# Kernel tuning notes

Measured on AMD Instinct MI355X. Metric: run time of the kernel, lower is better.

Reference implementation:

```python
import jax, jax.numpy as jnp
import numpy as np

N = 50000   # nodes
E = 800000  # edges
D = 128     # hidden_dim
O = 128     # out_dim (must equal hidden_dim; see prior_mean Linear)
T = 16      # number of timesteps for the modeled time encoding
EPS = 1e-9


def _gcn(x, W, b, src, dst, ew, n):
    """PyG-style GCNConv: add self-loops, symmetric deg^-1/2 normalization."""
    loop = jnp.arange(n)
    s = jnp.concatenate([src, loop])
    d = jnp.concatenate([dst, loop])
    w = jnp.concatenate([ew, jnp.ones((n,), x.dtype)])
    deg = jax.ops.segment_sum(w, d, num_segments=n)
    dinv = jnp.where(deg > 0, jax.lax.rsqrt(deg), 0.0)
    norm = dinv[s] * w * dinv[d]              # [E+N]
    h = x @ W                                  # [N, out]
    out = jax.ops.segment_sum(h[s] * norm[:, None], d, num_segments=n)
    return out + b


def setup_inputs() -> dict:
    key = jax.random.key(0)
    ks = jax.random.split(key, 20)

    def lin(k, fan_in, fan_out):
        return jax.random.normal(k, (fan_in, fan_out), jnp.float32) / np.sqrt(fan_in)

    return {
        "edge_index": jax.random.randint(ks[0], (2, E), 0, N, dtype=jnp.int64),
        "x": jax.random.normal(ks[1], (N, D), jnp.float32),
        "t": 3,
        "edge_score": jax.random.uniform(ks[2], (E,), jnp.float32),
        "total_len": 16,
        "train_len": 12,
        "W_enc": lin(ks[3], D, D), "b_enc": jnp.zeros((D,), jnp.float32),
        "W_mu": lin(ks[4], D, O), "b_mu": jnp.zeros((O,), jnp.float32),
        "W_std": lin(ks[5], D, O), "b_std": jnp.zeros((O,), jnp.float32),
        "W_prior": lin(ks[6], D, O), "b_prior": jnp.zeros((O,), jnp.float32),
        "W_pm": lin(ks[7], D, O), "b_pm": jnp.zeros((O,), jnp.float32),
        "W_ps": lin(ks[8], D, O), "b_ps": jnp.zeros((O,), jnp.float32),
        "time_emb": 0.02 * jax.random.normal(ks[9], (T, O), jnp.float32),
    }


def reference(edge_index, x, t, edge_score, total_len, train_len,
              W_enc, b_enc, W_mu, b_mu, W_std, b_std,
              W_prior, b_prior, W_pm, b_pm, W_ps, b_ps, time_emb):
    src, dst = edge_index[0], edge_index[1]
    n = x.shape[0]
    ones_e = jnp.ones((src.shape[0],), x.dtype)

    # encoder
    enc_t = jax.nn.relu(_gcn(x, W_enc, b_enc, src, dst, edge_score, n))
    # drop = 0.0 -> dropout is identity
    enc_mean_t = _gcn(enc_t, W_mu, b_mu, src, dst, ones_e, n)
    enc_std_t = jax.nn.sigmoid(_gcn(enc_t, W_std, b_std, src, dst, ones_e, n))

    # reparameterize (fixed eps for determinism)
    eps = jax.random.normal(jax.random.key(42), enc_mean_t.shape, enc_mean_t.dtype)
    conf_z_t = eps * enc_std_t + enc_mean_t

    # prior branch: time_encoding(prior, t) modeled as additive time embedding
    prior = jax.nn.relu(_gcn(x, W_prior, b_prior, src, dst, ones_e, n))
    prior = prior + time_emb[t]
    prior_mean = prior @ W_pm + b_pm
    prior_std = jax.nn.sigmoid(prior @ W_ps + b_ps)

    # fused KL divergence
    kl = (2.0 * jnp.log(prior_std + EPS) - 2.0 * jnp.log(enc_std_t + EPS)
          + ((enc_std_t + EPS) ** 2 + (enc_mean_t - prior_mean) ** 2)
          / (prior_std + EPS) ** 2 - 1.0)
    kl_loss = 0.5 * jnp.mean(jnp.sum(kl, axis=1), axis=0)
    return kl_loss, conf_z_t
```

## Files before the change

### kernel.cpp

```cpp
#include <hip/hip_runtime.h>
#include <math.h>

#define D 128

typedef unsigned int u32;
typedef unsigned short u16;
typedef __attribute__((ext_vector_type(8))) short bf16x8;
typedef __attribute__((ext_vector_type(4))) float f32x4;

__device__ __forceinline__ u32 rotl32(u32 x, int r){ return (x<<r) | (x>>(32-r)); }

__device__ __forceinline__ u16 f2bf(float x){
  u32 u = __float_as_uint(x);
  return (u16)((u + 0x7fffu + ((u >> 16) & 1u)) >> 16);
}
__device__ __forceinline__ float bf2f(u16 h){ return __uint_as_float(((u32)h) << 16); }

__device__ __forceinline__ float jax_normal_part_xor(u32 m){
  const u32 ks0 = 0u, ks1 = 42u, ks2 = 0x1BD11BF0u;
  u32 x0 = 0u + ks0;
  u32 x1 = m  + ks1;
  #define TF_R4(a,b,c,d) \
    x0 += x1; x1 = rotl32(x1,(a)); x1 ^= x0; \
    x0 += x1; x1 = rotl32(x1,(b)); x1 ^= x0; \
    x0 += x1; x1 = rotl32(x1,(c)); x1 ^= x0; \
    x0 += x1; x1 = rotl32(x1,(d)); x1 ^= x0;
  TF_R4(13,15,26,6)   x0 += ks1; x1 += ks2 + 1u;
  TF_R4(17,29,16,24)  x0 += ks2; x1 += ks0 + 2u;
  TF_R4(13,15,26,6)   x0 += ks0; x1 += ks1 + 3u;
  TF_R4(17,29,16,24)  x0 += ks1; x1 += ks2 + 4u;
  TF_R4(13,15,26,6)   x0 += ks2; x1 += ks0 + 5u;
  #undef TF_R4
  u32 bits = x0 ^ x1;
  float f = __uint_as_float((bits >> 9) | 0x3F800000u) - 1.0f;
  const float LO = -0.99999994f;
  float u = fmaxf(LO, f * 2.0f + LO);
  float w = -__logf(fmaf(-u, u, 1.0f));
  float p;
  if (w < 5.0f){
    w -= 2.5f;
    p =  2.81022636e-08f;
    p = fmaf(p, w,  3.43273939e-07f);
    p = fmaf(p, w, -3.5233877e-06f);
    p = fmaf(p, w, -4.39150654e-06f);
    p = fmaf(p, w,  0.00021858087f);
    p = fmaf(p, w, -0.00125372503f);
    p = fmaf(p, w, -0.00417768164f);
    p = fmaf(p, w,  0.246640727f);
    p = fmaf(p, w,  1.50140941f);
  } else {
    w = sqrtf(w) - 3.0f;
    p = -0.000200214257f;
    p = fmaf(p, w,  0.000100950558f);
    p = fmaf(p, w,  0.00134934322f);
    p = fmaf(p, w, -0.00367342844f);
    p = fmaf(p, w,  0.00573950773f);
    p = fmaf(p, w, -0.0076224613f);
    p = fmaf(p, w,  0.00943887047f);
    p = fmaf(p, w,  1.00167406f);
    p = fmaf(p, w,  2.83297682f);
  }
  return 1.41421354f * (p * u);
}

__device__ __forceinline__ float sigmoidf_(float z){ return 1.0f / (1.0f + __expf(-z)); }

__global__ __launch_bounds__(256) void k_eps(u32* __restrict__ epsb, int half_total){
  int idx = blockIdx.x*256 + threadIdx.x;
  int stride = gridDim.x*256;
  for (int i = idx; i < half_total; i += stride){
    u32 m0 = 2u*(u32)i;
    float e0 = jax_normal_part_xor(m0);
    float e1 = jax_normal_part_xor(m0 + 1u);
    epsb[i] = (u32)f2bf(e0) | ((u32)f2bf(e1) << 16);
  }
}

__global__ __launch_bounds__(256) void k_xconv(const float* __restrict__ x,
                                               u32* __restrict__ xb, int total2){
  int i = blockIdx.x*256 + threadIdx.x;
  if (i >= total2) return;
  float2 v = ((const float2*)x)[i];
  xb[i] = (u32)f2bf(v.x) | ((u32)f2bf(v.y) << 16);
}

__global__ void k_detect(const u32* __restrict__ e_u32, int* __restrict__ flag){
  __shared__ int s_nz;
  if (threadIdx.x == 0) s_nz = 0;
  __syncthreads();
  if (e_u32[2*threadIdx.x + 1] != 0u) atomicAdd(&s_nz, 1);
  __syncthreads();
  if (threadIdx.x == 0) *flag = (s_nz == 0) ? 1 : 0;
}

__global__ void k_init(int* __restrict__ cnt, int n){
  int i = blockIdx.x*256 + threadIdx.x;
  if (i < n) cnt[i] = 0;
}

__global__ void k_norm(const void* __restrict__ eidx, const int* __restrict__ flag,
                       int* __restrict__ src_w, int* __restrict__ dst_w,
                       int* __restrict__ cnt, int e){
  int i = blockIdx.x*256 + threadIdx.x;
  if (i >= e) return;
  int s, d;
  if (*flag){
    const u32* u = (const u32*)eidx;
    s = (int)u[2*(size_t)i];
    d = (int)u[2*((size_t)e + i)];
  } else {
    const int* p = (const int*)eidx;
    s = p[i];
    d = p[e + i];
  }
  src_w[i] = s;
  dst_w[i] = d;
  atomicAdd(&cnt[d], 1);
}

__global__ __launch_bounds__(256) void k_scan1(const int* __restrict__ cnt,
                                               int* __restrict__ rp,
                                               int* __restrict__ bsum, int n){
  __shared__ int sh[256];
  int tid = threadIdx.x, idx = blockIdx.x*256 + tid;
  int v = (idx < n) ? cnt[idx] : 0;
  sh[tid] = v; __syncthreads();
  for (int off = 1; off < 256; off <<= 1){
    int t = (tid >= off) ? sh[tid-off] : 0;
    __syncthreads(); sh[tid] += t; __syncthreads();
  }
  if (idx < n) rp[idx] = sh[tid] - v;
  if (tid == 255) bsum[blockIdx.x] = sh[255];
}

__global__ __launch_bounds__(1024) void k_scan2(int* __restrict__ bsum, int nb){
  __shared__ int sh[1024];
  int tid = threadIdx.x;
  int v = (tid < nb) ? bsum[tid] : 0;
  sh[tid] = v; __syncthreads();
  for (int off = 1; off < 1024; off <<= 1){
    int t = (tid >= off) ? sh[tid-off] : 0;
    __syncthreads(); sh[tid] += t; __syncthreads();
  }
  if (tid < nb) bsum[tid] = sh[tid] - v;
}

__global__ void k_scan3(int* __restrict__ rp, int* __restrict__ cur,
                        const int* __restrict__ bsum, const int* __restrict__ cnt,
                        float* __restrict__ dinv_o, int n, int e){
  int idx = blockIdx.x*256 + threadIdx.x;
  if (idx < n){
    int r = rp[idx] + bsum[blockIdx.x];
    rp[idx] = r; cur[idx] = r;
    dinv_o[idx] = rsqrtf((float)(cnt[idx] + 1));
  }
  if (idx == 0) rp[n] = e;
}

__global__ void k_scatter(const int* __restrict__ src, const int* __restrict__ dst,
                          const float* __restrict__ sc, int* __restrict__ cur,
                          int* __restrict__ col, float* __restrict__ wsrt, int e){
  int i = blockIdx.x*256 + threadIdx.x;
  if (i >= e) return;
  int d = dst[i];
  int p = atomicAdd(&cur[d], 1);
  col[p] = src[i];
  wsrt[p] = sc[i];
}

__global__ void k_deg(const int* __restrict__ rp, const float* __restrict__ wsrt,
                      float* __restrict__ dinv_s, int n){
  int i = blockIdx.x*256 + threadIdx.x;
  if (i >= n) return;
  float s = 1.0f;
  int e0 = rp[i], e1 = rp[i+1];
  for (int j = e0; j < e1; ++j) s += wsrt[j];
  dinv_s[i] = rsqrtf(s);
}

__global__ void k_wconv(const float* __restrict__ W0, const float* __restrict__ W1,
                        const float* __restrict__ W2, const float* __restrict__ W3,
                        const float* __restrict__ W4, const float* __restrict__ W5,
                        u16* __restrict__ wt){
  const float* Ws[6] = {W0,W1,W2,W3,W4,W5};
  const float* W = Ws[blockIdx.y];
  u16* Wt = wt + (size_t)blockIdx.y*16384;
  int idx = blockIdx.x*256 + threadIdx.x;
  int k = idx >> 7, col = idx & 127;
  Wt[col*128 + k] = f2bf(W[idx]);
}

__global__ __launch_bounds__(256) void k_agg_dual(
    const u32* __restrict__ xb, const int* __restrict__ rp,
    const int* __restrict__ col, const float* __restrict__ wsrt,
    const float* __restrict__ dinv_s, const float* __restrict__ dinv_o,
    u16* __restrict__ out_s, u16* __restrict__ out_o, int n){
  int wid = (blockIdx.x * 256 + threadIdx.x) >> 6;
  int lane = threadIdx.x & 63;
  if (wid >= n) return;
  float dsv = dinv_s[wid], dov = dinv_o[wid];
  u32 xv = xb[(size_t)wid*64 + lane];
  float xlo = bf2f((u16)(xv & 0xffff)), xhi = bf2f((u16)(xv >> 16));
  float ss = dsv*dsv, oo = dov*dov;
  float2 as = { xlo*ss, xhi*ss };
  float2 ao = { xlo*oo, xhi*oo };
  int e0 = rp[wid], e1 = rp[wid+1];
  for (int base = e0; base < e1; base += 64){
    int cnt = e1 - base; if (cnt > 64) cnt = 64;
    int idx = base + (lane < cnt ? lane : cnt - 1);
    int   sl = col[idx];
    float wl = wsrt[idx];
    float nsl = dinv_s[sl] * wl * dsv;
    float nol = dinv_o[sl] * dov;
    int j = 0;
    for (; j + 4 <= cnt; j += 4){
      int   s0=__shfl(sl,j),   s1=__shfl(sl,j+1),   s2=__shfl(sl,j+2),   s3=__shfl(sl,j+3);
      float a0=__shfl(nsl,j),  a1=__shfl(nsl,j+1),  a2=__shfl(nsl,j+2),  a3=__shfl(nsl,j+3);
      float b0=__shfl(nol,j),  b1=__shfl(nol,j+1),  b2=__shfl(nol,j+2),  b3=__shfl(nol,j+3);
      u32 r0 = xb[(size_t)s0*64 + lane];
      u32 r1 = xb[(size_t)s1*64 + lane];
      u32 r2 = xb[(size_t)s2*64 + lane];
      u32 r3 = xb[(size_t)s3*64 + lane];
      float l0 = bf2f((u16)(r0&0xffff)), h0 = bf2f((u16)(r0>>16));
      float l1 = bf2f((u16)(r1&0xffff)), h1 = bf2f((u16)(r1>>16));
      float l2 = bf2f((u16)(r2&0xffff)), h2 = bf2f((u16)(r2>>16));
      float l3 = bf2f((u16)(r3&0xffff)), h3 = bf2f((u16)(r3>>16));
      as.x = fmaf(a0,l0,as.x); as.y = fmaf(a0,h0,as.y);
      ao.x = fmaf(b0,l0,ao.x); ao.y = fmaf(b0,h0,ao.y);
      as.x = fmaf(a1,l1,as.x); as.y = fmaf(a1,h1,as.y);
      ao.x = fmaf(b1,l1,ao.x); ao.y = fmaf(b1,h1,ao.y);
      as.x = fmaf(a2,l2,as.x); as.y = fmaf(a2,h2,as.y);
      ao.x = fmaf(b2,l2,ao.x); ao.y = fmaf(b2,h2,ao.y);
      as.x = fmaf(a3,l3,as.x); as.y = fmaf(a3,h3,as.y);
      ao.x = fmaf(b3,l3,ao.x); ao.y = fmaf(b3,h3,ao.y);
    }
    for (; j < cnt; ++j){
      int   s0=__shfl(sl,j);
      float a0=__shfl(nsl,j), b0=__shfl(nol,j);
      u32 r0 = xb[(size_t)s0*64 + lane];
      float l0 = bf2f((u16)(r0&0xffff)), h0 = bf2f((u16)(r0>>16));
      as.x = fmaf(a0,l0,as.x); as.y = fmaf(a0,h0,as.y);
      ao.x = fmaf(b0,l0,ao.x); ao.y = fmaf(b0,h0,ao.y);
    }
  }
  ((u32*)out_s)[(size_t)wid*64 + lane] = (u32)f2bf(as.x) | ((u32)f2bf(as.y) << 16);
  ((u32*)out_o)[(size_t)wid*64 + lane] = (u32)f2bf(ao.x) | ((u32)f2bf(ao.y) << 16);
}

__global__ __launch_bounds__(256) void k_agg_one(
    const u16* __restrict__ h, const int* __restrict__ rp,
    const int* __restrict__ col, const float* __restrict__ dinv_o,
    u16* __restrict__ out, int n){
  int wid = (blockIdx.x * 256 + threadIdx.x) >> 6;
  int lane = threadIdx.x & 63;
  if (wid >= n) return;
  const u32* h2 = (const u32*)h;
  float dov = dinv_o[wid];
  u32 hv = h2[(size_t)wid*64 + lane];
  float oo = dov*dov;
  float2 ao = { bf2f((u16)(hv & 0xffff))*oo, bf2f((u16)(hv >> 16))*oo };
  int e0 = rp[wid], e1 = rp[wid+1];
  for (int base = e0; base < e1; base += 64){
    int cnt = e1 - base; if (cnt > 64) cnt = 64;
    int idx = base + (lane < cnt ? lane : cnt - 1);
    int   sl = col[idx];
    float nol = dinv_o[sl] * dov;
    int j = 0;
    for (; j + 4 <= cnt; j += 4){
      int   s0=__shfl(sl,j),  s1=__shfl(sl,j+1),  s2=__shfl(sl,j+2),  s3=__shfl(sl,j+3);
      float b0=__shfl(nol,j), b1=__shfl(nol,j+1), b2=__shfl(nol,j+2), b3=__shfl(nol,j+3);
      u32 r0 = h2[(size_t)s0*64 + lane];
      u32 r1 = h2[(size_t)s1*64 + lane];
      u32 r2 = h2[(size_t)s2*64 + lane];
      u32 r3 = h2[(size_t)s3*64 + lane];
      ao.x = fmaf(b0, bf2f((u16)(r0&0xffff)), ao.x); ao.y = fmaf(b0, bf2f((u16)(r0>>16)), ao.y);
      ao.x = fmaf(b1, bf2f((u16)(r1&0xffff)), ao.x); ao.y = fmaf(b1, bf2f((u16)(r1>>16)), ao.y);
      ao.x = fmaf(b2, bf2f((u16)(r2&0xffff)), ao.x); ao.y = fmaf(b2, bf2f((u16)(r2>>16)), ao.y);
      ao.x = fmaf(b3, bf2f((u16)(r3&0xffff)), ao.x); ao.y = fmaf(b3, bf2f((u16)(r3>>16)), ao.y);
    }
    for (; j < cnt; ++j){
      int   s0=__shfl(sl,j);
      float b0=__shfl(nol,j);
      u32 r0 = h2[(size_t)s0*64 + lane];
      ao.x = fmaf(b0, bf2f((u16)(r0&0xffff)), ao.x); ao.y = fmaf(b0, bf2f((u16)(r0>>16)), ao.y);
    }
  }
  ((u32*)out)[(size_t)wid*64 + lane] = (u32)f2bf(ao.x) | ((u32)f2bf(ao.y) << 16);
}


__global__ __launch_bounds__(256) void k_mfma_act2(
    const u16* __restrict__ A0, const u16* __restrict__ Wt0, const float* __restrict__ b0,
    const u16* __restrict__ A1, const u16* __restrict__ Wt1, const float* __restrict__ b1,
    const float* __restrict__ temb, const int* __restrict__ t_ptr,
    u16* __restrict__ out0, u16* __restrict__ out1, int n){
  const int sl = blockIdx.y;
  const u16* A  = sl ? A1 : A0;
  const u16* Wt = sl ? Wt1 : Wt0;
  const float* b = sl ? b1 : b0;
  u16* out = sl ? out1 : out0;
  const int tid = threadIdx.x;
  const int lane = tid & 63, wave = tid >> 6;
  const int lr = lane & 15, lg = lane >> 4;
  const int row0 = blockIdx.x * 16;
  int rowf = row0 + lr;
  int rowc = rowf < n ? rowf : n - 1;
  const char* Arow = (const char*)A + (size_t)rowc*256;
  const char* Wb   = (const char*)Wt + (wave*32 + lr)*256 + lg*16;
  f32x4 z = {0.f,0.f,0.f,0.f};
  f32x4 acc[2];
  acc[0] = z; acc[1] = z;
  #pragma unroll
  for (int ks = 0; ks < 4; ++ks){
    bf16x8 a = *(const bf16x8*)(Arow + ks*64 + lg*16);
    #pragma unroll
    for (int cf = 0; cf < 2; ++cf){
      bf16x8 bb = *(const bf16x8*)(Wb + cf*16*256 + ks*64);
      acc[cf] = __builtin_amdgcn_mfma_f32_16x16x32_bf16(a, bb, acc[cf], 0, 0, 0);
    }
  }
  int t = sl ? *t_ptr : 0;
  int rbase = row0 + (lg << 2);
  #pragma unroll
  for (int cf = 0; cf < 2; ++cf){
    int colw = wave*32 + cf*16 + lr;
    float bb = b[colw];
    float tt = sl ? temb[t*128 + colw] : 0.f;
    #pragma unroll
    for (int r = 0; r < 4; ++r){
      int row = rbase + r;
      if (row < n)
        out[(size_t)row*128 + colw] = f2bf(fmaxf(acc[cf][r] + bb, 0.f) + tt);
    }
  }
}

__global__ __launch_bounds__(256) void k_mfma_quad(
    const u16* __restrict__ Apr, const u16* __restrict__ Aen,
    const u16* __restrict__ Wtpm, const float* __restrict__ bpm,
    const u16* __restrict__ Wtps, const float* __restrict__ bps,
    const u16* __restrict__ Wtmu, const float* __restrict__ bmu,
    const u16* __restrict__ Wtsd, const float* __restrict__ bsd,
    const u32* __restrict__ epsb,
    float* __restrict__ conf, float* __restrict__ pblk, int n){
  const int tid = threadIdx.x;
  const int lane = tid & 63, wave = tid >> 6;
  const int lr = lane & 15, lg = lane >> 4;
  const int row0 = blockIdx.x * 16;
  int rowf = row0 + lr;
  int rowc = rowf < n ? rowf : n - 1;
  const char* Ap = (const char*)Apr + (size_t)rowc*256;
  const char* Ae = (const char*)Aen + (size_t)rowc*256;
  const int wcb = (wave*32 + lr)*256 + lg*16;
  const char* Wpm = (const char*)Wtpm + wcb;
  const char* Wps = (const char*)Wtps + wcb;
  const char* Wmu = (const char*)Wtmu + wcb;
  const char* Wsd = (const char*)Wtsd + wcb;
  int rbase = row0 + (lg << 2);
  u32 ew[2][4];
  #pragma unroll
  for (int cf = 0; cf < 2; ++cf){
    int colw = wave*32 + cf*16 + lr;
    #pragma unroll
    for (int r = 0; r < 4; ++r){
      int row = rbase + r; if (row >= n) row = n - 1;
      ew[cf][r] = epsb[(size_t)row*64 + (colw >> 1)];
    }
  }
  f32x4 z = {0.f,0.f,0.f,0.f};
  f32x4 aPM[2], aPS[2], aMU[2], aSD[2];
  #pragma unroll
  for (int i = 0; i < 2; ++i){ aPM[i]=z; aPS[i]=z; aMU[i]=z; aSD[i]=z; }
  #pragma unroll
  for (int ks = 0; ks < 4; ++ks){
    bf16x8 a5 = *(const bf16x8*)(Ap + ks*64 + lg*16);
    bf16x8 a2 = *(const bf16x8*)(Ae + ks*64 + lg*16);
    #pragma unroll
    for (int cf = 0; cf < 2; ++cf){
      int off = cf*16*256 + ks*64;
      aPM[cf] = __builtin_amdgcn_mfma_f32_16x16x32_bf16(a5, *(const bf16x8*)(Wpm+off), aPM[cf], 0,0,0);
      aPS[cf] = __builtin_amdgcn_mfma_f32_16x16x32_bf16(a5, *(const bf16x8*)(Wps+off), aPS[cf], 0,0,0);
      aMU[cf] = __builtin_amdgcn_mfma_f32_16x16x32_bf16(a2, *(const bf16x8*)(Wmu+off), aMU[cf], 0,0,0);
      aSD[cf] = __builtin_amdgcn_mfma_f32_16x16x32_bf16(a2, *(const bf16x8*)(Wsd+off), aSD[cf], 0,0,0);
    }
  }
  const float EPS = 1e-9f;
  float klsum = 0.f;
  #pragma unroll
  for (int cf = 0; cf < 2; ++cf){
    int colw = wave*32 + cf*16 + lr;
    float bb1 = bpm[colw], bb2 = bps[colw];
    float bb3 = bmu[colw], bb4 = bsd[colw];
    #pragma unroll
    for (int r = 0; r < 4; ++r){
      int row = rbase + r;
      if (row < n){
        size_t m = (size_t)row*128 + colw;
        float pmv = aPM[cf][r] + bb1;
        float psv = sigmoidf_(aPS[cf][r] + bb2);
        float em  = aMU[cf][r] + bb3;
        float es  = sigmoidf_(aSD[cf][r] + bb4);
        float eps = bf2f((u16)((colw & 1) ? (ew[cf][r] >> 16) : (ew[cf][r] & 0xffff)));
        conf[m] = fmaf(eps, es, em);
        float es_e = es + EPS, ps_e = psv + EPS;
        float diff = em - pmv;
        klsum += 2.0f*__logf(ps_e/es_e)
               + (es_e*es_e + diff*diff) / (ps_e*ps_e) - 1.0f;
      }
    }
  }
  #pragma unroll
  for (int off = 32; off > 0; off >>= 1) klsum += __shfl_down(klsum, off);
  __shared__ float wsum[4];
  if ((tid & 63) == 0) wsum[tid >> 6] = klsum;
  __syncthreads();
  if (tid == 0) pblk[blockIdx.x] = wsum[0] + wsum[1] + wsum[2] + wsum[3];
}

__global__ __launch_bounds__(256) void k_finish(const float* __restrict__ pblk, int nb,
                                                float* __restrict__ out0, int n){
  __shared__ double sh[256];
  double s = 0.0;
  for (int i = threadIdx.x; i < nb; i += 256) s += (double)pblk[i];
  sh[threadIdx.x] = s; __syncthreads();
  for (int off = 128; off > 0; off >>= 1){
    if (threadIdx.x < off) sh[threadIdx.x] += sh[threadIdx.x + off];
    __syncthreads();
  }
  if (threadIdx.x == 0) out0[0] = (float)(0.5 * sh[0] / (double)n);
}

extern "C" void kernel_launch(void* const* d_in, const int* in_sizes, int n_in,
                              void* d_out, int out_size, void* d_ws, size_t ws_size,
                              hipStream_t stream){
  const void*  eidx   = d_in[0];
  const float* x      = (const float*)d_in[1];
  const int*   t_ptr  = (const int*)d_in[2];
  const float* escore = (const float*)d_in[3];
  const float* W_enc = (const float*)d_in[6];  const float* b_enc = (const float*)d_in[7];
  const float* W_mu  = (const float*)d_in[8];  const float* b_mu  = (const float*)d_in[9];
  const float* W_std = (const float*)d_in[10]; const float* b_std = (const float*)d_in[11];
  const float* W_pr  = (const float*)d_in[12]; const float* b_pr  = (const float*)d_in[13];
  const float* W_pm  = (const float*)d_in[14]; const float* b_pm  = (const float*)d_in[15];
  const float* W_ps  = (const float*)d_in[16]; const float* b_ps  = (const float*)d_in[17];
  const float* temb  = (const float*)d_in[18];

  const int N = in_sizes[1] / D;
  const int E = in_sizes[3];

  char* w = (char*)d_ws;
  auto alloc = [&](size_t bytes) -> char* {
    char* p = w; w += (bytes + 255) & ~(size_t)255; return p;
  };
  int*    flag   = (int*)   alloc(256);
  int*    src_w  = (int*)   alloc((size_t)E*4);
  int*    dst_w  = (int*)   alloc((size_t)E*4);
  int*    cnt    = (int*)   alloc((size_t)N*4);
  int*    rp     = (int*)   alloc((size_t)(N+1)*4);
  int*    cur    = (int*)   alloc((size_t)N*4);
  float*  dinv_s = (float*) alloc((size_t)N*4);
  float*  dinv_o = (float*) alloc((size_t)N*4);
  int*    bsum   = (int*)   alloc(1024*4);
  int*    col    = (int*)   alloc((size_t)E*4);
  float*  wsrt   = (float*) alloc((size_t)E*4);
  u16*    wt     = (u16*)   alloc((size_t)6*16384*2);
  u32*    XB     = (u32*)   alloc((size_t)N*64*4);
  u16*    B1     = (u16*)   alloc((size_t)N*D*2);
  u16*    B2     = (u16*)   alloc((size_t)N*D*2);
  u16*    B3     = (u16*)   alloc((size_t)N*D*2);
  u16*    B5     = (u16*)   alloc((size_t)N*D*2);
  u32*    EPSB   = (u32*)   alloc((size_t)N*64*4);
  const int gG16 = (N + 15) / 16;
  float*  pblk   = (float*) alloc((size_t)gG16*4);
  (void)ws_size; (void)n_in; (void)out_size;

  float* conf = ((float*)d_out) + 1;

  u16* Wt_enc = wt + 0*16384;
  u16* Wt_pr  = wt + 1*16384;
  u16* Wt_pm  = wt + 2*16384;
  u16* Wt_ps  = wt + 3*16384;
  u16* Wt_mu  = wt + 4*16384;
  u16* Wt_std = wt + 5*16384;

  const int gE  = (E + 255) / 256;
  const int gN  = (N + 255) / 256;
  const int gW  = (N * 64 + 255) / 256;

  k_eps    <<<2048, 256, 0, stream>>>(EPSB, N*64);
  k_xconv  <<<gW, 256, 0, stream>>>(x, XB, N*64);
  k_wconv  <<<dim3(64,6), 256, 0, stream>>>(W_enc, W_pr, W_pm, W_ps, W_mu, W_std, wt);
  k_detect <<<1, 256, 0, stream>>>((const u32*)eidx, flag);
  k_init   <<<gN, 256, 0, stream>>>(cnt, N);
  k_norm   <<<gE, 256, 0, stream>>>(eidx, flag, src_w, dst_w, cnt, E);
  k_scan1  <<<gN, 256, 0, stream>>>(cnt, rp, bsum, N);
  k_scan2  <<<1, 1024, 0, stream>>>(bsum, gN);
  k_scan3  <<<gN, 256, 0, stream>>>(rp, cur, bsum, cnt, dinv_o, N, E);
  k_scatter<<<gE, 256, 0, stream>>>(src_w, dst_w, escore, cur, col, wsrt, E);
  k_deg    <<<gN, 256, 0, stream>>>(rp, wsrt, dinv_s, N);

  k_agg_dual<<<gW, 256, 0, stream>>>(XB, rp, col, wsrt, dinv_s, dinv_o, B1, B2, N);
  k_mfma_act2<<<dim3(gG16,2), 256, 0, stream>>>(B1, Wt_enc, b_enc, B2, Wt_pr, b_pr,
                                                temb, t_ptr, B3, B5, N);
  k_agg_one<<<gW, 256, 0, stream>>>(B3, rp, col, dinv_o, B2, N);
  k_mfma_quad<<<gG16, 256, 0, stream>>>(B5, B2, Wt_pm, b_pm, Wt_ps, b_ps,
                                        Wt_mu, b_mu, Wt_std, b_std, EPSB,
                                        conf, pblk, N);
  k_finish<<<1, 256, 0, stream>>>(pblk, gG16, (float*)d_out, N);
}
```

Before: 326.3 us.

## Merge prep kernels into one launch and compute weighted degree via atomics

Folds the eps generation, x-to-bf16 conversion, weight transpose/convert and index-dtype detection into a single k_prep launch that partitions work by block index. Count zeroing moves to hipMemsetAsync. Weighted degree is now accumulated with float atomics in a new k_degacc pass, with dinv_s computed in scan3, replacing the per-node serial k_deg loop over sorted weights. This removes several small launches and the load-imbalanced degree loop, at the cost of an extra edge pass with atomic contention and float-atomic summation order nondeterminism.

```diff
diff --git a/kernel.cpp b/kernel.cpp
--- a/kernel.cpp
+++ b/kernel.cpp
@@ -65,10 +65,43 @@
 
 __device__ __forceinline__ float sigmoidf_(float z){ return 1.0f / (1.0f + __expf(-z)); }
 
-__global__ __launch_bounds__(256) void k_eps(u32* __restrict__ epsb, int half_total){
-  int idx = blockIdx.x*256 + threadIdx.x;
-  int stride = gridDim.x*256;
-  for (int i = idx; i < half_total; i += stride){
+__global__ __launch_bounds__(256) void k_prep(
+    const u32* __restrict__ e_u32, int* __restrict__ flag,
+    const float* __restrict__ W0, const float* __restrict__ W1,
+    const float* __restrict__ W2, const float* __restrict__ W3,
+    const float* __restrict__ W4, const float* __restrict__ W5,
+    u16* __restrict__ wt,
+    const float* __restrict__ x, u32* __restrict__ xb, int nx2,
+    u32* __restrict__ epsb, int neps2, int nxb){
+  const int bid = blockIdx.x, tid = threadIdx.x;
+  if (bid == 0){
+    __shared__ int s_nz;
+    if (tid == 0) s_nz = 0;
+    __syncthreads();
+    if (e_u32[2*tid + 1] != 0u) atomicAdd(&s_nz, 1);
+    __syncthreads();
+    if (tid == 0) *flag = (s_nz == 0) ? 1 : 0;
+    return;
+  }
+  if (bid <= 384){
+    int gid = (bid-1)*256 + tid;
+    const float* Ws[6] = {W0,W1,W2,W3,W4,W5};
+    int mat = gid >> 14, idx = gid & 16383;
+    int k = idx >> 7, col = idx & 127;
+    wt[mat*16384 + col*128 + k] = f2bf(Ws[mat][idx]);
+    return;
+  }
+  if (bid <= 384 + nxb){
+    int i = (bid - 385)*256 + tid;
+    if (i < nx2){
+      float2 v = ((const float2*)x)[i];
+      xb[i] = (u32)f2bf(v.x) | ((u32)f2bf(v.y) << 16);
+    }
+    return;
+  }
+  int base = 385 + nxb;
+  int estride = (gridDim.x - base) * 256;
+  for (int i = (bid - base)*256 + tid; i < neps2; i += estride){
     u32 m0 = 2u*(u32)i;
     float e0 = jax_normal_part_xor(m0);
     float e1 = jax_normal_part_xor(m0 + 1u);
@@ -76,31 +109,9 @@
   }
 }
 
-__global__ __launch_bounds__(256) void k_xconv(const float* __restrict__ x,
-                                               u32* __restrict__ xb, int total2){
-  int i = blockIdx.x*256 + threadIdx.x;
-  if (i >= total2) return;
-  float2 v = ((const float2*)x)[i];
-  xb[i] = (u32)f2bf(v.x) | ((u32)f2bf(v.y) << 16);
-}
-
-__global__ void k_detect(const u32* __restrict__ e_u32, int* __restrict__ flag){
-  __shared__ int s_nz;
-  if (threadIdx.x == 0) s_nz = 0;
-  __syncthreads();
-  if (e_u32[2*threadIdx.x + 1] != 0u) atomicAdd(&s_nz, 1);
-  __syncthreads();
-  if (threadIdx.x == 0) *flag = (s_nz == 0) ? 1 : 0;
-}
-
-__global__ void k_init(int* __restrict__ cnt, int n){
-  int i = blockIdx.x*256 + threadIdx.x;
-  if (i < n) cnt[i] = 0;
-}
-
 __global__ void k_norm(const void* __restrict__ eidx, const int* __restrict__ flag,
                        int* __restrict__ src_w, int* __restrict__ dst_w,
-                       int* __restrict__ cnt, int e){
+                       int* __restrict__ cnt, float* __restrict__ degsc, int e){
   int i = blockIdx.x*256 + threadIdx.x;
   if (i >= e) return;
   int s, d;
@@ -118,6 +129,13 @@
   atomicAdd(&cnt[d], 1);
 }
 
+__global__ void k_degacc(const int* __restrict__ dst, const float* __restrict__ sc,
+                         float* __restrict__ degsc, int e){
+  int i = blockIdx.x*256 + threadIdx.x;
+  if (i >= e) return;
+  unsafeAtomicAdd(&degsc[dst[i]], sc[i]);
+}
+
 __global__ __launch_bounds__(256) void k_scan1(const int* __restrict__ cnt,
                                                int* __restrict__ rp,
                                                int* __restrict__ bsum, int n){
@@ -147,12 +165,15 @@
 
 __global__ void k_scan3(int* __restrict__ rp, int* __restrict__ cur,
                         const int* __restrict__ bsum, const int* __restrict__ cnt,
-                        float* __restrict__ dinv_o, int n, int e){
+                        const float* __restrict__ degsc,
+                        float* __restrict__ dinv_s, float* __restrict__ dinv_o,
+                        int n, int e){
   int idx = blockIdx.x*256 + threadIdx.x;
   if (idx < n){
     int r = rp[idx] + bsum[blockIdx.x];
     rp[idx] = r; cur[idx] = r;
     dinv_o[idx] = rsqrtf((float)(cnt[idx] + 1));
+    dinv_s[idx] = rsqrtf(1.0f + degsc[idx]);
   }
   if (idx == 0) rp[n] = e;
 }
@@ -166,28 +187,6 @@
   int p = atomicAdd(&cur[d], 1);
   col[p] = src[i];
   wsrt[p] = sc[i];
-}
-
-__global__ void k_deg(const int* __restrict__ rp, const float* __restrict__ wsrt,
-                      float* __restrict__ dinv_s, int n){
-  int i = blockIdx.x*256 + threadIdx.x;
-  if (i >= n) return;
-  float s = 1.0f;
-  int e0 = rp[i], e1 = rp[i+1];
-  for (int j = e0; j < e1; ++j) s += wsrt[j];
-  dinv_s[i] = rsqrtf(s);
-}
-
-__global__ void k_wconv(const float* __restrict__ W0, const float* __restrict__ W1,
-                        const float* __restrict__ W2, const float* __restrict__ W3,
-                        const float* __restrict__ W4, const float* __restrict__ W5,
-                        u16* __restrict__ wt){
-  const float* Ws[6] = {W0,W1,W2,W3,W4,W5};
-  const float* W = Ws[blockIdx.y];
-  u16* Wt = wt + (size_t)blockIdx.y*16384;
-  int idx = blockIdx.x*256 + threadIdx.x;
-  int k = idx >> 7, col = idx & 127;
-  Wt[col*128 + k] = f2bf(W[idx]);
 }
 
 __global__ __launch_bounds__(256) void k_agg_dual(
@@ -458,6 +457,7 @@
   int*    cnt    = (int*)   alloc((size_t)N*4);
   int*    rp     = (int*)   alloc((size_t)(N+1)*4);
   int*    cur    = (int*)   alloc((size_t)N*4);
+  float*  degsc  = (float*) alloc((size_t)N*4);
   float*  dinv_s = (float*) alloc((size_t)N*4);
   float*  dinv_o = (float*) alloc((size_t)N*4);
   int*    bsum   = (int*)   alloc(1024*4);
@@ -487,17 +487,19 @@
   const int gN  = (N + 255) / 256;
   const int gW  = (N * 64 + 255) / 256;
 
-  k_eps    <<<2048, 256, 0, stream>>>(EPSB, N*64);
-  k_xconv  <<<gW, 256, 0, stream>>>(x, XB, N*64);
-  k_wconv  <<<dim3(64,6), 256, 0, stream>>>(W_enc, W_pr, W_pm, W_ps, W_mu, W_std, wt);
-  k_detect <<<1, 256, 0, stream>>>((const u32*)eidx, flag);
-  k_init   <<<gN, 256, 0, stream>>>(cnt, N);
-  k_norm   <<<gE, 256, 0, stream>>>(eidx, flag, src_w, dst_w, cnt, E);
+  hipMemsetAsync(cnt, 0, (size_t)N*4, stream);
+  hipMemsetAsync(degsc, 0, (size_t)N*4, stream);
+
+  k_prep<<<1 + 384 + gW + 2048, 256, 0, stream>>>(
+      (const u32*)eidx, flag, W_enc, W_pr, W_pm, W_ps, W_mu, W_std, wt,
+      x, XB, N*64, EPSB, N*64, gW);
+
+  k_norm   <<<gE, 256, 0, stream>>>(eidx, flag, src_w, dst_w, cnt, degsc, E);
+  k_degacc <<<gE, 256, 0, stream>>>(dst_w, escore, degsc, E);
   k_scan1  <<<gN, 256, 0, stream>>>(cnt, rp, bsum, N);
   k_scan2  <<<1, 1024, 0, stream>>>(bsum, gN);
-  k_scan3  <<<gN, 256, 0, stream>>>(rp, cur, bsum, cnt, dinv_o, N, E);
+  k_scan3  <<<gN, 256, 0, stream>>>(rp, cur, bsum, cnt, degsc, dinv_s, dinv_o, N, E);
   k_scatter<<<gE, 256, 0, stream>>>(src_w, dst_w, escore, cur, col, wsrt, E);
-  k_deg    <<<gN, 256, 0, stream>>>(rp, wsrt, dinv_s, N);
 
   k_agg_dual<<<gW, 256, 0, stream>>>(XB, rp, col, wsrt, dinv_s, dinv_o, B1, B2, N);
   k_mfma_act2<<<dim3(gG16,2), 256, 0, stream>>>(B1, Wt_enc, b_enc, B2, Wt_pr, b_pr,
```

Measured after the change: 366.0 us. 1.12x slower.
